# Kernel tuning notes

Measured on AMD Instinct MI355X. Metric: run time of the kernel, lower is better.

Reference implementation:

```python
import jax, jax.numpy as jnp
import numpy as np

D_MODEL = 1024
H = 16
D_K = D_MODEL // H
B = 128   # batch (intersample attention attends across this dim)
N = 256   # samples / tokens per row


def setup_inputs() -> dict:
    key = jax.random.key(0)
    ks = jax.random.split(key, 8)
    s = 1.0 / np.sqrt(D_MODEL)
    return {
        "query": jax.random.normal(ks[0], (B, N, D_MODEL), jnp.float32),
        "key":   jax.random.normal(ks[1], (B, N, D_MODEL), jnp.float32),
        "value": jax.random.normal(ks[2], (B, N, D_MODEL), jnp.float32),
        "Wq": jax.random.normal(ks[3], (D_MODEL, D_MODEL), jnp.float32) * s,
        "bq": jnp.zeros((D_MODEL,), jnp.float32),
        "Wk": jax.random.normal(ks[4], (D_MODEL, D_MODEL), jnp.float32) * s,
        "bk": jnp.zeros((D_MODEL,), jnp.float32),
        "Wv": jax.random.normal(ks[5], (D_MODEL, D_MODEL), jnp.float32) * s,
        "bv": jnp.zeros((D_MODEL,), jnp.float32),
        "Wo": jax.random.normal(ks[6], (D_MODEL, D_MODEL), jnp.float32) * s,
        "bo": jnp.zeros((D_MODEL,), jnp.float32),
    }


def _proj_heads(x, W, b):
    # torch nn.Linear: x @ W.T + b ; then view (b, n, h, d_k) -> (b, h, n, d_k)
    y = jnp.einsum('bnd,ed->bne', x, W) + b
    bsz, n, _ = y.shape
    return y.reshape(bsz, n, H, D_K).transpose(0, 2, 1, 3)


def reference(query, key, value, Wq, bq, Wk, bk, Wv, bv, Wo, bo):
    q = _proj_heads(query, Wq, bq)  # (b, h, n, d_k)
    k = _proj_heads(key,   Wk, bk)
    v = _proj_heads(value, Wv, bv)
    # intersample attention: attend ACROSS the batch dim b (per head, per sample n)
    scale = 1.0 / jnp.sqrt(jnp.asarray(D_K, q.dtype))
    scores = jnp.einsum('bhnd,chnd->hnbc', q, k) * scale  # (h, n, b, b)
    p = jax.nn.softmax(scores, axis=-1)
    out = jnp.einsum('hnbc,chnd->bhnd', p, v)             # (b, h, n, d_k)
    # merge heads: (b, h, n, d_k) -> (b, n, h*d_k)
    bsz, _, n, _ = out.shape
    out = out.transpose(0, 2, 1, 3).reshape(bsz, n, H * D_K)
    return jnp.einsum('bnd,ed->bne', out, Wo) + bo
```

## Files before the change

### kernel.cpp

```cpp
#include <hip/hip_runtime.h>
#include <hip/hip_bf16.h>
#include <stdint.h>

#define D_MODEL 1024
#define HEADS   16
#define DK      64
#define BATCH   128
#define NTOK    256
#define MROWS   (BATCH * NTOK)

typedef __attribute__((ext_vector_type(8))) short bf16x8;
typedef __attribute__((ext_vector_type(4))) float f32x4;

__device__ __forceinline__ unsigned short f2b_rne(float f) {
    union { float f; unsigned int u; } c; c.f = f;
    unsigned int u = c.u;
    unsigned int r = (u + 0x7FFFu + ((u >> 16) & 1u)) >> 16;
    return (unsigned short)r;
}

__device__ __forceinline__ void async16(const void* g, void* l) {
    __builtin_amdgcn_global_load_lds(
        (__attribute__((address_space(1))) void*)g,
        (__attribute__((address_space(3))) void*)l,
        16, 0, 0);
}

__global__ __launch_bounds__(256)
void f2b_kernel(const float* __restrict__ x, ushort* __restrict__ y, int n4) {
    int i = blockIdx.x * blockDim.x + threadIdx.x;
    int stride = gridDim.x * blockDim.x;
    for (; i < n4; i += stride) {
        float4 v = ((const float4*)x)[i];
        ushort4 o;
        o.x = f2b_rne(v.x); o.y = f2b_rne(v.y);
        o.z = f2b_rne(v.z); o.w = f2b_rne(v.w);
        ((ushort4*)y)[i] = o;
    }
}

template<int MODE>
__global__ __launch_bounds__(512, 2)
void gemm_nt(const ushort* __restrict__ A, const ushort* __restrict__ B,
             const float* __restrict__ bias, void* __restrict__ Cout,
             int M, int N, int K, float alpha)
{
    __shared__ ushort smem[65536];

    const int tid  = threadIdx.x;
    const int wave = tid >> 6, lane = tid & 63;
    const int quad = lane >> 4, l15 = lane & 15;
    const int swz  = l15 & 7;

    const int o  = blockIdx.x;
    const int s  = (o & 7) * 64 + (o >> 3);
    const int pm = (s >> 2) * 256;
    const int pn = (s & 3) * 256;

    const int arow = (wave >> 2) * 128;
    const int brow = (wave & 3) * 64;

    const size_t laneoff = (size_t)(lane >> 3) * K
                         + (size_t)(((lane & 7) ^ (lane >> 3)) << 3);
    const ushort* Ab = A + (size_t)(pm + wave * 32) * K + laneoff;
    const ushort* Bb = B + (size_t)(pn + wave * 32) * K + laneoff;

    f32x4 acc[8][4] = {};
    bf16x8 afrag[4], bfrag[4];

#define STAGE(BUF, kt) do {                                                     \
    const ushort* ag_ = Ab + (size_t)(kt) * 64;                                 \
    const ushort* bg_ = Bb + (size_t)(kt) * 64;                                 \
    _Pragma("unroll")                                                           \
    for (int i_ = 0; i_ < 4; ++i_) {                                            \
        async16(ag_ + (size_t)(i_ * 8) * K,                                     \
                &smem[(BUF) * 32768 + wave * 2048 + i_ * 512]);                 \
        async16(bg_ + (size_t)(i_ * 8) * K,                                     \
                &smem[(BUF) * 32768 + 16384 + wave * 2048 + i_ * 512]);         \
    }                                                                           \
} while (0)

#define LDB(BUF, kkidx) do {                                                    \
    _Pragma("unroll")                                                           \
    for (int n_ = 0; n_ < 4; ++n_)                                              \
        bfrag[n_] = *(const bf16x8*)&smem[(BUF) * 32768 + 16384                 \
            + (brow + n_ * 16 + l15) * 64                                       \
            + ((((kkidx) * 4 + quad) ^ swz) << 3)];                             \
} while (0)

#define LDA(BUF, kkidx, qm) do {                                                \
    _Pragma("unroll")                                                           \
    for (int m_ = 0; m_ < 4; ++m_)                                              \
        afrag[m_] = *(const bf16x8*)&smem[(BUF) * 32768                         \
            + (arow + ((qm) * 4 + m_) * 16 + l15) * 64                          \
            + ((((kkidx) * 4 + quad) ^ swz) << 3)];                             \
} while (0)

#define MFMA16(qm) do {                                                         \
    __builtin_amdgcn_s_setprio(1);                                              \
    _Pragma("unroll")                                                           \
    for (int m_ = 0; m_ < 4; ++m_)                                              \
        _Pragma("unroll")                                                       \
        for (int n_ = 0; n_ < 4; ++n_)                                          \
            acc[(qm) * 4 + m_][n_] = __builtin_amdgcn_mfma_f32_16x16x32_bf16(   \
                afrag[m_], bfrag[n_], acc[(qm) * 4 + m_][n_], 0, 0, 0);         \
    __builtin_amdgcn_s_setprio(0);                                              \
} while (0)

#define PHASE_STD(BUF, kkidx, qm, RB) do {                                      \
    if (RB) LDB(BUF, kkidx);                                                    \
    LDA(BUF, kkidx, qm);                                                        \
    __builtin_amdgcn_s_barrier();                                               \
    asm volatile("s_waitcnt lgkmcnt(0)" ::: "memory");                          \
    __builtin_amdgcn_sched_barrier(0);                                          \
    MFMA16(qm);                                                                 \
    __builtin_amdgcn_s_barrier();                                               \
} while (0)

#define PHASE_LAST(BUF, kt, vmN) do {                                           \
    LDA(BUF, 1, 1);                                                             \
    asm volatile("s_waitcnt lgkmcnt(0)" ::: "memory");                          \
    __builtin_amdgcn_sched_barrier(0);                                          \
    __builtin_amdgcn_s_barrier();                                               \
    if ((kt) >= 0) STAGE(BUF, kt);                                              \
    MFMA16(1);                                                                  \
    if ((vmN) == 8)      { asm volatile("s_waitcnt vmcnt(8)" ::: "memory"); }   \
    else if ((vmN) == 0) { asm volatile("s_waitcnt vmcnt(0)" ::: "memory"); }   \
    __builtin_amdgcn_sched_barrier(0);                                          \
    __builtin_amdgcn_s_barrier();                                               \
} while (0)

    STAGE(0, 0);
    STAGE(1, 1);
    asm volatile("s_waitcnt vmcnt(8)" ::: "memory");
    __builtin_amdgcn_sched_barrier(0);
    __builtin_amdgcn_s_barrier();

    #pragma unroll 1
    for (int it = 0; it < 8; ++it) {
        const int t2 = 2 * it + 2;
        const int t3 = 2 * it + 3;
        PHASE_STD(0, 0, 0, 1);
        PHASE_STD(0, 0, 1, 0);
        PHASE_STD(0, 1, 0, 1);
        PHASE_LAST(0, (t2 < 16) ? t2 : -1, (t2 < 16) ? 8 : 0);
        PHASE_STD(1, 0, 0, 1);
        PHASE_STD(1, 0, 1, 0);
        PHASE_STD(1, 1, 0, 1);
        PHASE_LAST(1, (t3 < 16) ? t3 : -1, (t3 < 16) ? 8 : -1);
    }

#undef PHASE_LAST
#undef PHASE_STD
#undef MFMA16
#undef LDA
#undef LDB
#undef STAGE

    if (MODE == 0) {
        ushort* out = (ushort*)Cout;
        #pragma unroll
        for (int m = 0; m < 8; ++m) {
            const int mbase = pm + arow + m * 16 + quad * 4;
            #pragma unroll
            for (int n = 0; n < 4; ++n) {
                const int e = pn + brow + n * 16 + l15;
                const float bv = bias[e];
                const int h = e >> 6, d = e & 63;
                #pragma unroll
                for (int r = 0; r < 4; ++r) {
                    const int mm = mbase + r;
                    const int bb = mm >> 8, nn = mm & 255;
                    float val = (acc[m][n][r] + bv) * alpha;
                    out[(size_t)(((h << 8) + nn) * 128 + bb) * 64 + d] = f2b_rne(val);
                }
            }
        }
    } else {
        float* out = (float*)Cout;
        #pragma unroll
        for (int m = 0; m < 8; ++m) {
            const int mbase = pm + arow + m * 16 + quad * 4;
            #pragma unroll
            for (int n = 0; n < 4; ++n) {
                const int e = pn + brow + n * 16 + l15;
                const float bv = bias[e];
                #pragma unroll
                for (int r = 0; r < 4; ++r) {
                    const int mm = mbase + r;
                    out[(size_t)mm * N + e] = acc[m][n][r] + bv;
                }
            }
        }
    }
}

__global__ __launch_bounds__(256)
void attn_kernel(const ushort* __restrict__ Qp, const ushort* __restrict__ Kp,
                 const ushort* __restrict__ Vp, ushort* __restrict__ Ob)
{
    __shared__ ushort sm[24576];

    const int tid  = threadIdx.x;
    const int wave = tid >> 6, lane = tid & 63;
    const int quad = lane >> 4, l15 = lane & 15;
    const int hn = blockIdx.x;
    const int h = hn >> 8, n = hn & 255;
    const size_t base = (size_t)hn * (BATCH * DK);

    {
        const uint4* Qg = (const uint4*)(Qp + base);
        const uint4* Kg = (const uint4*)(Kp + base);
        uint4* s4 = (uint4*)sm;
        #pragma unroll
        for (int i = 0; i < 4; i++) {
            int id = tid + i * 256;
            s4[id]        = Qg[id];
            s4[1024 + id] = Kg[id];
        }
        const uint4* Vg = (const uint4*)(Vp + base);
        #pragma unroll
        for (int i = 0; i < 4; i++) {
            int id = tid + i * 256;
            int c = id >> 3, d8 = (id & 7) * 8;
            uint4 vv = Vg[id];
            const ushort* vs = (const ushort*)&vv;
            #pragma unroll
            for (int j = 0; j < 8; j++)
                sm[16384 + (d8 + j) * 128 + c] = vs[j];
        }
    }
    __syncthreads();

    f32x4 accs[2][8] = {};
    #pragma unroll
    for (int kk = 0; kk < 64; kk += 32) {
        bf16x8 aq[2], bk8[8];
        #pragma unroll
        for (int mt = 0; mt < 2; mt++)
            aq[mt] = *(const bf16x8*)&sm[(wave * 32 + mt * 16 + l15) * 64 + kk + quad * 8];
        #pragma unroll
        for (int nt = 0; nt < 8; nt++)
            bk8[nt] = *(const bf16x8*)&sm[8192 + (nt * 16 + l15) * 64 + kk + quad * 8];
        #pragma unroll
        for (int mt = 0; mt < 2; mt++)
            #pragma unroll
            for (int nt = 0; nt < 8; nt++)
                accs[mt][nt] = __builtin_amdgcn_mfma_f32_16x16x32_bf16(aq[mt], bk8[nt], accs[mt][nt], 0, 0, 0);
    }

    #pragma unroll
    for (int mt = 0; mt < 2; mt++) {
        #pragma unroll
        for (int r = 0; r < 4; r++) {
            float mx = accs[mt][0][r];
            #pragma unroll
            for (int nt = 1; nt < 8; nt++) mx = fmaxf(mx, accs[mt][nt][r]);
            #pragma unroll
            for (int s = 1; s < 16; s <<= 1) mx = fmaxf(mx, __shfl_xor(mx, s, 64));
            float sum = 0.f;
            #pragma unroll
            for (int nt = 0; nt < 8; nt++) {
                float e = __expf(accs[mt][nt][r] - mx);
                accs[mt][nt][r] = e;
                sum += e;
            }
            #pragma unroll
            for (int s = 1; s < 16; s <<= 1) sum += __shfl_xor(sum, s, 64);
            float inv = 1.0f / sum;
            #pragma unroll
            for (int nt = 0; nt < 8; nt++) accs[mt][nt][r] *= inv;
        }
    }

    __syncthreads();

    #pragma unroll
    for (int mt = 0; mt < 2; mt++)
        #pragma unroll
        for (int nt = 0; nt < 8; nt++)
            #pragma unroll
            for (int r = 0; r < 4; r++)
                sm[(wave * 32 + mt * 16 + quad * 4 + r) * 128 + nt * 16 + l15] =
                    f2b_rne(accs[mt][nt][r]);
    __syncthreads();

    f32x4 acco[2][4] = {};
    #pragma unroll
    for (int kk = 0; kk < 128; kk += 32) {
        bf16x8 ap[2], bv8[4];
        #pragma unroll
        for (int mt = 0; mt < 2; mt++)
            ap[mt] = *(const bf16x8*)&sm[(wave * 32 + mt * 16 + l15) * 128 + kk + quad * 8];
        #pragma unroll
        for (int nt = 0; nt < 4; nt++)
            bv8[nt] = *(const bf16x8*)&sm[16384 + (nt * 16 + l15) * 128 + kk + quad * 8];
        #pragma unroll
        for (int mt = 0; mt < 2; mt++)
            #pragma unroll
            for (int nt = 0; nt < 4; nt++)
                acco[mt][nt] = __builtin_amdgcn_mfma_f32_16x16x32_bf16(ap[mt], bv8[nt], acco[mt][nt], 0, 0, 0);
    }

    #pragma unroll
    for (int mt = 0; mt < 2; mt++)
        #pragma unroll
        for (int nt = 0; nt < 4; nt++)
            #pragma unroll
            for (int r = 0; r < 4; r++) {
                int b = wave * 32 + mt * 16 + quad * 4 + r;
                int d = nt * 16 + l15;
                Ob[((size_t)b * NTOK + n) * D_MODEL + h * DK + d] = f2b_rne(acco[mt][nt][r]);
            }
}

extern "C" void kernel_launch(void* const* d_in, const int* in_sizes, int n_in,
                              void* d_out, int out_size, void* d_ws, size_t ws_size,
                              hipStream_t stream)
{
    const float* q  = (const float*)d_in[0];
    const float* k  = (const float*)d_in[1];
    const float* v  = (const float*)d_in[2];
    const float* Wq = (const float*)d_in[3];
    const float* bq = (const float*)d_in[4];
    const float* Wk = (const float*)d_in[5];
    const float* bk = (const float*)d_in[6];
    const float* Wv = (const float*)d_in[7];
    const float* bv = (const float*)d_in[8];
    const float* Wo = (const float*)d_in[9];
    const float* bo = (const float*)d_in[10];

    const int XE = MROWS * D_MODEL;
    const int WE = D_MODEL * D_MODEL;

    ushort* xb = (ushort*)d_ws;
    ushort* Kp = xb + (size_t)XE;
    ushort* Vp = Kp + (size_t)XE;
    ushort* Wb = Vp + (size_t)XE;
    ushort* Qp = (ushort*)d_out;

    dim3 blk(256);
    dim3 gblk(512);
    dim3 ggemm(512);

    f2b_kernel<<<dim3(512),  blk, 0, stream>>>(Wq, Wb + 0 * (size_t)WE, WE / 4);
    f2b_kernel<<<dim3(512),  blk, 0, stream>>>(Wk, Wb + 1 * (size_t)WE, WE / 4);
    f2b_kernel<<<dim3(512),  blk, 0, stream>>>(Wv, Wb + 2 * (size_t)WE, WE / 4);
    f2b_kernel<<<dim3(512),  blk, 0, stream>>>(Wo, Wb + 3 * (size_t)WE, WE / 4);

    f2b_kernel<<<dim3(4096), blk, 0, stream>>>(q, xb, XE / 4);
    gemm_nt<0><<<ggemm, gblk, 0, stream>>>(xb, Wb + 0 * (size_t)WE, bq, Qp,
                                           MROWS, D_MODEL, D_MODEL, 0.125f);
    f2b_kernel<<<dim3(4096), blk, 0, stream>>>(k, xb, XE / 4);
    gemm_nt<0><<<ggemm, gblk, 0, stream>>>(xb, Wb + 1 * (size_t)WE, bk, Kp,
                                           MROWS, D_MODEL, D_MODEL, 1.0f);
    f2b_kernel<<<dim3(4096), blk, 0, stream>>>(v, xb, XE / 4);
    gemm_nt<0><<<ggemm, gblk, 0, stream>>>(xb, Wb + 2 * (size_t)WE, bv, Vp,
                                           MROWS, D_MODEL, D_MODEL, 1.0f);

    attn_kernel<<<dim3(HEADS * NTOK), blk, 0, stream>>>(Qp, Kp, Vp, xb);

    gemm_nt<1><<<ggemm, gblk, 0, stream>>>(xb, Wb + 3 * (size_t)WE, bo, d_out,
                                           MROWS, D_MODEL, D_MODEL, 1.0f);
}
```

Before: 820.3 us.

## Write V transposed from projection GEMM, swizzle attention LDS, batch conversion launches

The V projection GEMM now writes V directly in a (h,n,d,b) transposed layout, so the attention kernel no longer does a scalar scatter-transpose into LDS. Q, K, V and P tiles in LDS use an XOR swizzle to cut bank conflicts, and the MFMA loops are bracketed with s_setprio. The weight conversions are merged into one launch, and the q and k input conversions are merged into another, using spare space in the output buffer to hold the converted k. The transposed V store from the GEMM is strided by 128 elements, which may make that epilogue slower.

```diff
diff --git a/kernel.cpp b/kernel.cpp
--- a/kernel.cpp
+++ b/kernel.cpp
@@ -32,6 +32,40 @@
     int stride = gridDim.x * blockDim.x;
     for (; i < n4; i += stride) {
         float4 v = ((const float4*)x)[i];
+        ushort4 o;
+        o.x = f2b_rne(v.x); o.y = f2b_rne(v.y);
+        o.z = f2b_rne(v.z); o.w = f2b_rne(v.w);
+        ((ushort4*)y)[i] = o;
+    }
+}
+
+__global__ __launch_bounds__(256)
+void f2b2_kernel(const float* __restrict__ xa, const float* __restrict__ xc,
+                 ushort* __restrict__ ya, ushort* __restrict__ yc, int n4) {
+    int i = blockIdx.x * blockDim.x + threadIdx.x;
+    int stride = gridDim.x * blockDim.x;
+    for (; i < 2 * n4; i += stride) {
+        const float* src = (i < n4) ? xa : xc;
+        ushort*      dst = (i < n4) ? ya : yc;
+        int j = (i < n4) ? i : i - n4;
+        float4 v = ((const float4*)src)[j];
+        ushort4 o;
+        o.x = f2b_rne(v.x); o.y = f2b_rne(v.y);
+        o.z = f2b_rne(v.z); o.w = f2b_rne(v.w);
+        ((ushort4*)dst)[j] = o;
+    }
+}
+
+__global__ __launch_bounds__(256)
+void f2b4_kernel(const float* __restrict__ w0, const float* __restrict__ w1,
+                 const float* __restrict__ w2, const float* __restrict__ w3,
+                 ushort* __restrict__ y, int n4) {
+    int i = blockIdx.x * blockDim.x + threadIdx.x;
+    int stride = gridDim.x * blockDim.x;
+    for (; i < 4 * n4; i += stride) {
+        int sel = i / n4, j = i & (n4 - 1);
+        const float* src = (sel == 0) ? w0 : (sel == 1) ? w1 : (sel == 2) ? w2 : w3;
+        float4 v = ((const float4*)src)[j];
         ushort4 o;
         o.x = f2b_rne(v.x); o.y = f2b_rne(v.y);
         o.z = f2b_rne(v.z); o.w = f2b_rne(v.w);
@@ -157,7 +191,7 @@
 #undef LDB
 #undef STAGE
 
-    if (MODE == 0) {
+    if (MODE == 0 || MODE == 2) {
         ushort* out = (ushort*)Cout;
         #pragma unroll
         for (int m = 0; m < 8; ++m) {
@@ -172,7 +206,10 @@
                     const int mm = mbase + r;
                     const int bb = mm >> 8, nn = mm & 255;
                     float val = (acc[m][n][r] + bv) * alpha;
-                    out[(size_t)(((h << 8) + nn) * 128 + bb) * 64 + d] = f2b_rne(val);
+                    size_t idx = (MODE == 0)
+                        ? ((size_t)(((h << 8) + nn) * 128 + bb) * 64 + d)
+                        : ((size_t)(((h << 8) + nn) * 64 + d) * 128 + bb);
+                    out[idx] = f2b_rne(val);
                 }
             }
         }
@@ -199,11 +236,12 @@
 void attn_kernel(const ushort* __restrict__ Qp, const ushort* __restrict__ Kp,
                  const ushort* __restrict__ Vp, ushort* __restrict__ Ob)
 {
-    __shared__ ushort sm[24576];
+    __shared__ __align__(16) ushort sm[24576];
 
     const int tid  = threadIdx.x;
     const int wave = tid >> 6, lane = tid & 63;
     const int quad = lane >> 4, l15 = lane & 15;
+    const int sw   = l15 & 7;
     const int hn = blockIdx.x;
     const int h = hn >> 8, n = hn & 255;
     const size_t base = (size_t)hn * (BATCH * DK);
@@ -211,42 +249,40 @@
     {
         const uint4* Qg = (const uint4*)(Qp + base);
         const uint4* Kg = (const uint4*)(Kp + base);
+        const uint4* Vg = (const uint4*)(Vp + base);
         uint4* s4 = (uint4*)sm;
         #pragma unroll
         for (int i = 0; i < 4; i++) {
             int id = tid + i * 256;
-            s4[id]        = Qg[id];
-            s4[1024 + id] = Kg[id];
-        }
-        const uint4* Vg = (const uint4*)(Vp + base);
-        #pragma unroll
-        for (int i = 0; i < 4; i++) {
-            int id = tid + i * 256;
-            int c = id >> 3, d8 = (id & 7) * 8;
-            uint4 vv = Vg[id];
-            const ushort* vs = (const ushort*)&vv;
-            #pragma unroll
-            for (int j = 0; j < 8; j++)
-                sm[16384 + (d8 + j) * 128 + c] = vs[j];
+            int qr = id >> 3, qs = id & 7;
+            int ql = qr * 8 + (qs ^ (qr & 7));
+            s4[ql]        = Qg[id];
+            s4[1024 + ql] = Kg[id];
+            int vr = id >> 4, vs = id & 15;
+            s4[2048 + vr * 16 + (vs ^ (vr & 7))] = Vg[id];
         }
     }
     __syncthreads();
 
     f32x4 accs[2][8] = {};
     #pragma unroll
-    for (int kk = 0; kk < 64; kk += 32) {
+    for (int kh = 0; kh < 2; kh++) {
         bf16x8 aq[2], bk8[8];
         #pragma unroll
         for (int mt = 0; mt < 2; mt++)
-            aq[mt] = *(const bf16x8*)&sm[(wave * 32 + mt * 16 + l15) * 64 + kk + quad * 8];
+            aq[mt] = *(const bf16x8*)&sm[(wave * 32 + mt * 16 + l15) * 64
+                                         + (((kh * 4 + quad) ^ sw) << 3)];
         #pragma unroll
         for (int nt = 0; nt < 8; nt++)
-            bk8[nt] = *(const bf16x8*)&sm[8192 + (nt * 16 + l15) * 64 + kk + quad * 8];
+            bk8[nt] = *(const bf16x8*)&sm[8192 + (nt * 16 + l15) * 64
+                                          + (((kh * 4 + quad) ^ sw) << 3)];
+        __builtin_amdgcn_s_setprio(1);
         #pragma unroll
         for (int mt = 0; mt < 2; mt++)
             #pragma unroll
             for (int nt = 0; nt < 8; nt++)
                 accs[mt][nt] = __builtin_amdgcn_mfma_f32_16x16x32_bf16(aq[mt], bk8[nt], accs[mt][nt], 0, 0, 0);
+        __builtin_amdgcn_s_setprio(0);
     }
 
     #pragma unroll
@@ -280,26 +316,32 @@
         #pragma unroll
         for (int nt = 0; nt < 8; nt++)
             #pragma unroll
-            for (int r = 0; r < 4; r++)
-                sm[(wave * 32 + mt * 16 + quad * 4 + r) * 128 + nt * 16 + l15] =
+            for (int r = 0; r < 4; r++) {
+                int rw = wave * 32 + mt * 16 + quad * 4 + r;
+                sm[rw * 128 + (((nt * 2 + (l15 >> 3)) ^ (rw & 7)) << 3) + (l15 & 7)] =
                     f2b_rne(accs[mt][nt][r]);
+            }
     __syncthreads();
 
     f32x4 acco[2][4] = {};
     #pragma unroll
-    for (int kk = 0; kk < 128; kk += 32) {
+    for (int kh = 0; kh < 4; kh++) {
         bf16x8 ap[2], bv8[4];
         #pragma unroll
         for (int mt = 0; mt < 2; mt++)
-            ap[mt] = *(const bf16x8*)&sm[(wave * 32 + mt * 16 + l15) * 128 + kk + quad * 8];
+            ap[mt] = *(const bf16x8*)&sm[(wave * 32 + mt * 16 + l15) * 128
+                                         + (((kh * 4 + quad) ^ sw) << 3)];
         #pragma unroll
         for (int nt = 0; nt < 4; nt++)
-            bv8[nt] = *(const bf16x8*)&sm[16384 + (nt * 16 + l15) * 128 + kk + quad * 8];
+            bv8[nt] = *(const bf16x8*)&sm[16384 + (nt * 16 + l15) * 128
+                                          + (((kh * 4 + quad) ^ sw) << 3)];
+        __builtin_amdgcn_s_setprio(1);
         #pragma unroll
         for (int mt = 0; mt < 2; mt++)
             #pragma unroll
             for (int nt = 0; nt < 4; nt++)
                 acco[mt][nt] = __builtin_amdgcn_mfma_f32_16x16x32_bf16(ap[mt], bv8[nt], acco[mt][nt], 0, 0, 0);
+        __builtin_amdgcn_s_setprio(0);
     }
 
     #pragma unroll
@@ -338,24 +380,22 @@
     ushort* Vp = Kp + (size_t)XE;
     ushort* Wb = Vp + (size_t)XE;
     ushort* Qp = (ushort*)d_out;
+    ushort* kb = Qp + (size_t)XE;
 
     dim3 blk(256);
     dim3 gblk(512);
     dim3 ggemm(512);
 
-    f2b_kernel<<<dim3(512),  blk, 0, stream>>>(Wq, Wb + 0 * (size_t)WE, WE / 4);
-    f2b_kernel<<<dim3(512),  blk, 0, stream>>>(Wk, Wb + 1 * (size_t)WE, WE / 4);
-    f2b_kernel<<<dim3(512),  blk, 0, stream>>>(Wv, Wb + 2 * (size_t)WE, WE / 4);
-    f2b_kernel<<<dim3(512),  blk, 0, stream>>>(Wo, Wb + 3 * (size_t)WE, WE / 4);
-
-    f2b_kernel<<<dim3(4096), blk, 0, stream>>>(q, xb, XE / 4);
+    f2b4_kernel<<<dim3(1024), blk, 0, stream>>>(Wq, Wk, Wv, Wo, Wb, WE / 4);
+
+    f2b2_kernel<<<dim3(4096), blk, 0, stream>>>(q, k, xb, kb, XE / 4);
+
     gemm_nt<0><<<ggemm, gblk, 0, stream>>>(xb, Wb + 0 * (size_t)WE, bq, Qp,
                                            MROWS, D_MODEL, D_MODEL, 0.125f);
-    f2b_kernel<<<dim3(4096), blk, 0, stream>>>(k, xb, XE / 4);
-    gemm_nt<0><<<ggemm, gblk, 0, stream>>>(xb, Wb + 1 * (size_t)WE, bk, Kp,
+    gemm_nt<0><<<ggemm, gblk, 0, stream>>>(kb, Wb + 1 * (size_t)WE, bk, Kp,
                                            MROWS, D_MODEL, D_MODEL, 1.0f);
     f2b_kernel<<<dim3(4096), blk, 0, stream>>>(v, xb, XE / 4);
-    gemm_nt<0><<<ggemm, gblk, 0, stream>>>(xb, Wb + 2 * (size_t)WE, bv, Vp,
+    gemm_nt<2><<<ggemm, gblk, 0, stream>>>(xb, Wb + 2 * (size_t)WE, bv, Vp,
                                            MROWS, D_MODEL, D_MODEL, 1.0f);
 
     attn_kernel<<<dim3(HEADS * NTOK), blk, 0, stream>>>(Qp, Kp, Vp, xb);
```

After: 947.5 us. 1.16x slower.
